# Optimization experiments

Measured on AMD Instinct MI355X. Metric: run time of the kernel, lower is better.

Reference implementation:

```python
import jax, jax.numpy as jnp
import numpy as np

B, T, C = 8, 2048, 1024
H, D = 16, 64
DLOW = 64  # D_DECAY = D_AAA = D_MV = D_GATE = 64
EPS_LN = 1e-5


def setup_inputs() -> dict:
    key = jax.random.key(0)
    ks = jax.random.split(key, 26)
    p = lambda k, shape, s=0.02: (jax.random.normal(k, shape, jnp.float32) * s)
    u = lambda k, shape: jax.random.uniform(k, shape, jnp.float32)
    return {
        "x":   jax.random.normal(ks[0], (B, T, C), jnp.float32),
        # token-shift mix coefficients (1,1,C)
        "x_r": u(ks[1], (1, 1, C)), "x_w": u(ks[2], (1, 1, C)),
        "x_k": u(ks[3], (1, 1, C)), "x_v": u(ks[4], (1, 1, C)),
        "x_a": u(ks[5], (1, 1, C)), "x_g": u(ks[6], (1, 1, C)),
        # decay lora: w1 [C,DLOW], w2 [DLOW,H], w0 [1,1,H,1]
        "w0": p(ks[7], (1, 1, H, 1)), "w1": p(ks[8], (C, DLOW)), "w2": p(ks[9], (DLOW, H)),
        # in-context lr lora
        "a0": p(ks[10], (1, 1, H, 1)), "a1": p(ks[11], (C, DLOW)), "a2": p(ks[12], (DLOW, H)),
        # value residual lora
        "v0": p(ks[13], (1, 1, C)), "v1": p(ks[14], (C, DLOW)), "v2": p(ks[15], (DLOW, C)),
        # gate lora
        "g1": p(ks[16], (C, DLOW)), "g2": p(ks[17], (DLOW, C)),
        "k_k": 0.85 + p(ks[18], (1, 1, C)),
        "r_k": p(ks[19], (H, D)),
        # main projections, stored [in, out] so x @ W matches nn.Linear
        "Wr": p(ks[20], (C, C)), "Wk": p(ks[21], (C, C)),
        "Wv": p(ks[22], (C, C)), "Wo": p(ks[23], (C, C)),
        # GroupNorm(n_head, n_embd) affine params
        "ln_w": jnp.ones((C,), jnp.float32) + p(ks[24], (C,)),
        "ln_b": p(ks[25], (C,)),
    }


def reference(x, x_r, x_w, x_k, x_v, x_a, x_g,
              w0, w1, w2, a0, a1, a2, v0, v1, v2, g1, g2,
              k_k, r_k, Wr, Wk, Wv, Wo, ln_w, ln_b):
    Bb, Tt, Cc = x.shape
    Hh, Dd = r_k.shape
    # token shift: sx = x_t - x_{t-1} (zero-padded)
    xx = jnp.concatenate([jnp.zeros((Bb, 1, Cc), x.dtype), x[:, :-1]], axis=1)
    sx = x - xx
    xr = x + sx * x_r
    xw = x + sx * x_w
    xk = x + sx * x_k
    xv = x + sx * x_v
    xa = x + sx * x_a
    xg = x + sx * x_g

    r = (xr @ Wr).reshape(Bb, Tt, Hh, Dd)
    # decay in (0, exp(-0.5)): exp(-softplus(-(w0 + lora)) - 0.5)
    w = jnp.exp(-jax.nn.softplus(-(w0 + (jnp.tanh(xw @ w1) @ w2).reshape(Bb, Tt, Hh, 1))) - 0.5)
    k = xk @ Wk
    v = xv @ Wv
    v_res_gate = jax.nn.sigmoid(v0 + jnp.tanh(xv @ v1) @ v2)
    v = v + (v - v) * v_res_gate  # no-op, kept for faithfulness
    a = jax.nn.sigmoid(a0 + (jnp.tanh(xa @ a1) @ a2).reshape(Bb, Tt, Hh, 1))
    g = jax.nn.sigmoid(jnp.tanh(xg @ g1) @ g2)

    kk = (k * k_k).reshape(Bb, Tt, Hh, Dd)
    kk = kk / jnp.maximum(jnp.linalg.norm(kk, axis=-1, keepdims=True), 1e-12)
    vh = v.reshape(Bb, Tt, Hh, Dd)

    # WKV linear recurrence: state = state * w_t + kk_t * v_t * a_t
    kv = (kk * vh * a).astype(jnp.float32)            # [B,T,H,D]
    w_t = jnp.moveaxis(w.astype(jnp.float32), 1, 0)   # [T,B,H,1]
    kv_t = jnp.moveaxis(kv, 1, 0)                     # [T,B,H,D]

    def step(state, inputs):
        wt, kvt = inputs
        state = state * wt + kvt
        return state, state

    init = jnp.zeros((Bb, Hh, Dd), jnp.float32)
    _, states = jax.lax.scan(step, init, (w_t, kv_t))  # [T,B,H,D]
    x_wkv = jnp.moveaxis(states, 0, 1).astype(x.dtype)  # [B,T,H,D]

    x_wkv = x_wkv * r
    bonus = jnp.sum(r * kk * r_k, axis=-1, keepdims=True) * vh
    x_wkv = x_wkv + bonus  # [B,T,H,D]

    # GroupNorm(H groups over C channels), per (B*T) sample
    mean = x_wkv.mean(axis=-1, keepdims=True)
    var = x_wkv.var(axis=-1, keepdims=True)
    xn = (x_wkv - mean) * jax.lax.rsqrt(var + EPS_LN)
    xn = xn.reshape(Bb, Tt, Cc) * ln_w + ln_b

    return (xn * g) @ Wo
```

## Files before the change

kernel.cpp:

```cpp
#include <hip/hip_runtime.h>


typedef __bf16 bf16;
typedef __attribute__((ext_vector_type(8))) __bf16 bf16x8;
typedef __attribute__((ext_vector_type(4))) float f32x4;

#define TBTOK 16384
#define TSEQ  2048
#define CDIM  1024
#define HN    16
#define CHUNK 32
#define NCH   64

__device__ __forceinline__ float wredsum(float v) {
#pragma unroll
  for (int o = 32; o > 0; o >>= 1) v += __shfl_xor(v, o, 64);
  return v;
}
__device__ __forceinline__ float redsum8(float v) {
#pragma unroll
  for (int o = 4; o > 0; o >>= 1) v += __shfl_xor(v, o, 64);
  return v;
}
__device__ __forceinline__ float sigmf(float x) { return 1.f / (1.f + expf(-x)); }

__device__ __forceinline__ void gl_lds16(const bf16* g, bf16* l) {
  __builtin_amdgcn_global_load_lds(
      (const __attribute__((address_space(1))) unsigned int*)g,
      (__attribute__((address_space(3))) unsigned int*)l, 16, 0, 0);
}

__global__ __launch_bounds__(256) void prep_kern(
    const float* __restrict__ x, const float* __restrict__ mr,
    const float* __restrict__ mk, const float* __restrict__ mv,
    bf16* __restrict__ xr, bf16* __restrict__ xk, bf16* __restrict__ xv,
    bf16* __restrict__ xbf,
    const float* __restrict__ Wr, const float* __restrict__ Wk,
    const float* __restrict__ Wv, const float* __restrict__ Wo,
    const float* __restrict__ w1, const float* __restrict__ a1, const float* __restrict__ g1,
    const float* __restrict__ mw, const float* __restrict__ ma, const float* __restrict__ mg,
    const float* __restrict__ g2, const float* __restrict__ w2, const float* __restrict__ a2,
    bf16* __restrict__ WrT, bf16* __restrict__ WkT, bf16* __restrict__ WvT, bf16* __restrict__ WoT,
    bf16* __restrict__ Bcat, bf16* __restrict__ g2T,
    bf16* __restrict__ w2T, bf16* __restrict__ a2T, float* __restrict__ zpad) {
  int bid0 = blockIdx.x;
  int tid = threadIdx.x;
  if (bid0 < 8192) {
    long i8 = ((long)bid0 * 256 + tid) * 8;
    int m = (int)(i8 >> 10);
    int c = (int)(i8 & 1023);
    f32x4 x0 = *(const f32x4*)(x + i8);
    f32x4 x1 = *(const f32x4*)(x + i8 + 4);
    f32x4 p0 = {0.f, 0.f, 0.f, 0.f}, p1 = {0.f, 0.f, 0.f, 0.f};
    if ((m & (TSEQ - 1)) != 0) {
      p0 = *(const f32x4*)(x + i8 - CDIM);
      p1 = *(const f32x4*)(x + i8 - CDIM + 4);
    }
    f32x4 r0 = *(const f32x4*)(mr + c), r1 = *(const f32x4*)(mr + c + 4);
    f32x4 k0 = *(const f32x4*)(mk + c), k1 = *(const f32x4*)(mk + c + 4);
    f32x4 v0 = *(const f32x4*)(mv + c), v1 = *(const f32x4*)(mv + c + 4);
    bf16x8 or_, ok_, ov_, ox_;
#pragma unroll
    for (int j = 0; j < 4; j++) {
      float s0 = x0[j] - p0[j], s1 = x1[j] - p1[j];
      or_[j] = (bf16)(x0[j] + s0 * r0[j]); or_[4 + j] = (bf16)(x1[j] + s1 * r1[j]);
      ok_[j] = (bf16)(x0[j] + s0 * k0[j]); ok_[4 + j] = (bf16)(x1[j] + s1 * k1[j]);
      ov_[j] = (bf16)(x0[j] + s0 * v0[j]); ov_[4 + j] = (bf16)(x1[j] + s1 * v1[j]);
      ox_[j] = (bf16)x0[j];                ox_[4 + j] = (bf16)x1[j];
    }
    *(bf16x8*)(xr + i8) = or_;
    *(bf16x8*)(xk + i8) = ok_;
    *(bf16x8*)(xv + i8) = ov_;
    *(bf16x8*)(xbf + i8) = ox_;
    return;
  }
  int bid = bid0 - 8192;
  int tx = tid & 31, ty = tid >> 5;
  __shared__ bf16 tile[32][33];
  if (bid < 4096) {
    int sel = bid >> 10, t = bid & 1023;
    int k0 = (t >> 5) * 32, n0 = (t & 31) * 32;
    const float* src = sel == 0 ? Wr : (sel == 1 ? Wk : (sel == 2 ? Wv : Wo));
    bf16* dst = sel == 0 ? WrT : (sel == 1 ? WkT : (sel == 2 ? WvT : WoT));
#pragma unroll
    for (int i = 0; i < 4; i++)
      tile[ty + i * 8][tx] = (bf16)src[(long)(k0 + ty + i * 8) * 1024 + n0 + tx];
    __syncthreads();
#pragma unroll
    for (int i = 0; i < 4; i++)
      dst[(long)(n0 + ty + i * 8) * 1024 + k0 + tx] = tile[tx][ty + i * 8];
  } else if (bid < 4480) {
    int idx = bid - 4096;
    int mat = idx >> 7, rem = idx & 127;
    int half = rem >> 6, t = rem & 63;
    int k0 = (t >> 1) * 32, n0 = (t & 1) * 32;
    const float* W = mat == 0 ? w1 : (mat == 1 ? a1 : g1);
    const float* mx = mat == 0 ? mw : (mat == 1 ? ma : mg);
#pragma unroll
    for (int i = 0; i < 4; i++) {
      int k = k0 + ty + i * 8;
      float s = half == 0 ? (1.f + mx[k]) : (-mx[k]);
      tile[ty + i * 8][tx] = (bf16)(s * W[(long)k * 64 + n0 + tx]);
    }
    __syncthreads();
#pragma unroll
    for (int i = 0; i < 4; i++)
      Bcat[(long)(mat * 64 + n0 + ty + i * 8) * 2048 + half * 1024 + k0 + tx] =
          tile[tx][ty + i * 8];
  } else if (bid < 4544) {
    int t = bid - 4480;
    int k0 = (t >> 5) * 32, n0 = (t & 31) * 32;
#pragma unroll
    for (int i = 0; i < 4; i++)
      tile[ty + i * 8][tx] = (bf16)g2[(long)(k0 + ty + i * 8) * 1024 + n0 + tx];
    __syncthreads();
#pragma unroll
    for (int i = 0; i < 4; i++)
      g2T[(long)(n0 + ty + i * 8) * 64 + k0 + tx] = tile[tx][ty + i * 8];
  } else {
#pragma unroll
    for (int rep = 0; rep < 4; rep++) {
      int idx = rep * 256 + tid;
      int k = idx >> 4, h = idx & 15;
      w2T[h * 64 + k] = (bf16)w2[idx];
      a2T[h * 64 + k] = (bf16)a2[idx];
    }
    if (tid < 64) zpad[tid] = 0.f;
  }
}

#define BARRIER __builtin_amdgcn_s_barrier()
#define LGKM0                                              \
  do {                                                     \
    asm volatile("s_waitcnt lgkmcnt(0)" ::: "memory");     \
    __builtin_amdgcn_sched_barrier(0);                     \
  } while (0)

#define READ_A(HALFP, QM)                                                                \
  {                                                                                      \
    const bf16* _h = (HALFP);                                                            \
    _Pragma("unroll") for (int i = 0; i < 4; i++) {                                      \
      int ra = (QM)*64 + i * 16 + lr;                                                    \
      _Pragma("unroll") for (int ks = 0; ks < 2; ks++)                                   \
          af[i][ks] = *(const bf16x8*)&_h[ra * 64 + (((ks * 4 + quad) ^ (ra & 7)) * 8)]; \
    }                                                                                    \
  }

#define READ_B(HALFP, QN)                                                                \
  {                                                                                      \
    const bf16* _h = (HALFP);                                                            \
    _Pragma("unroll") for (int jj = 0; jj < 2; jj++) {                                   \
      int rb = bro + ((QN)*2 + jj) * 16 + lr;                                            \
      _Pragma("unroll") for (int ks = 0; ks < 2; ks++)                                   \
          bfr[(QN)*2 + jj][ks] =                                                         \
              *(const bf16x8*)&_h[rb * 64 + (((ks * 4 + quad) ^ (rb & 7)) * 8)];         \
    }                                                                                    \
  }

#define MFMA16(QM, QN)                                                            \
  __builtin_amdgcn_s_setprio(1);                                                  \
  _Pragma("unroll") for (int ks = 0; ks < 2; ks++)                                \
  _Pragma("unroll") for (int i = 0; i < 4; i++)                                   \
  _Pragma("unroll") for (int jj = 0; jj < 2; jj++)                                \
      acc[(QM)*4 + i][(QN)*2 + jj] = __builtin_amdgcn_mfma_f32_16x16x32_bf16(     \
          af[i][ks], bfr[(QN)*2 + jj][ks], acc[(QM)*4 + i][(QN)*2 + jj], 0, 0, 0);\
  __builtin_amdgcn_s_setprio(0);

template <typename OT>
__global__ __launch_bounds__(512, 2) void gemm256_kern(
    const bf16* __restrict__ A0, const bf16* __restrict__ A1, const bf16* __restrict__ A2,
    const bf16* __restrict__ BT0, const bf16* __restrict__ BT1, const bf16* __restrict__ BT2,
    OT* __restrict__ out0, OT* __restrict__ out1, OT* __restrict__ out2,
    int K, int nbpm) {
  int nwg = gridDim.x;
  int id = blockIdx.x;
  int qq = nwg >> 3;
  int wg = (id & 7) * qq + (id >> 3);
  int mat = wg / nbpm;
  int rem = wg - mat * nbpm;
  int m0 = (rem & 63) << 8;
  int n0 = (rem >> 6) << 8;
  const bf16* Am = mat == 0 ? A0 : (mat == 1 ? A1 : A2);
  const bf16* BTm = mat == 0 ? BT0 : (mat == 1 ? BT1 : BT2);
  OT* out = mat == 0 ? out0 : (mat == 1 ? out1 : out2);

  __shared__ bf16 Al[2][2][128 * 64];
  __shared__ bf16 Bl[2][2][128 * 64];

  int tid = threadIdx.x;
  int w = tid >> 6, lane = tid & 63, quad = lane >> 4, lr = lane & 15;
  int wr = w >> 2, wc = w & 3;
  int hb = wc >> 1, bro = (wc & 1) * 64;

  int swz = ((tid & 7) ^ ((tid >> 3) & 7)) * 8;
  const bf16* aBase = Am + (long)(m0 + (tid >> 3)) * K + swz;
  const bf16* bBase = BTm + (long)(n0 + (tid >> 3)) * K + swz;

  auto stgA = [&](int db, int h, int t) {
    const bf16* g = aBase + (long)(h * 128) * K + t * 64;
    bf16* l = &Al[db][h][0] + w * 512;
    gl_lds16(g, l);
    gl_lds16(g + (long)64 * K, l + 4096);
  };
  auto stgB = [&](int db, int h, int t) {
    const bf16* g = bBase + (long)(h * 128) * K + t * 64;
    bf16* l = &Bl[db][h][0] + w * 512;
    gl_lds16(g, l);
    gl_lds16(g + (long)64 * K, l + 4096);
  };

  const bf16* A0p = &Al[0][wr][0];
  const bf16* A1p = &Al[1][wr][0];
  const bf16* B0p = &Bl[0][hb][0];
  const bf16* B1p = &Bl[1][hb][0];

  f32x4 acc[8][4] = {};
  bf16x8 af[4][2], bfr[4][2];

  int NT = K >> 6, NU = NT >> 1;

  stgB(0, 0, 0); stgA(0, 0, 0); stgA(0, 1, 0); stgB(0, 1, 0);
  stgB(1, 0, 1); stgA(1, 0, 1);
  asm volatile("s_waitcnt vmcnt(4)" ::: "memory");
  BARRIER;

#pragma unroll 1
  for (int u = 0; u < NU; u++) {
    int t1 = 2 * u + 1, t2 = 2 * u + 2, t3 = 2 * u + 3;
    READ_A(A0p, 0);
    READ_B(B0p, 0);
    stgA(1, 1, t1);
    asm volatile("s_waitcnt lgkmcnt(8)" ::: "memory");
    BARRIER; LGKM0;
    MFMA16(0, 0);
    BARRIER;
    READ_B(B0p, 1);
    stgB(1, 1, t1);
    BARRIER; LGKM0;
    MFMA16(0, 1);
    BARRIER;
    READ_A(A0p, 1);
    if (t2 < NT) stgB(0, 0, t2);
    BARRIER; LGKM0;
    MFMA16(1, 1);
    BARRIER;
    if (t2 < NT) stgA(0, 0, t2);
    BARRIER;
    __builtin_amdgcn_sched_barrier(0);
    MFMA16(1, 0);
    if (t2 < NT) { asm volatile("s_waitcnt vmcnt(4)" ::: "memory"); }
    else         { asm volatile("s_waitcnt vmcnt(0)" ::: "memory"); }
    BARRIER;
    READ_A(A1p, 0);
    READ_B(B1p, 0);
    if (t2 < NT) stgA(0, 1, t2);
    asm volatile("s_waitcnt lgkmcnt(8)" ::: "memory");
    BARRIER; LGKM0;
    MFMA16(0, 0);
    BARRIER;
    READ_B(B1p, 1);
    if (t2 < NT) stgB(0, 1, t2);
    BARRIER; LGKM0;
    MFMA16(0, 1);
    BARRIER;
    READ_A(A1p, 1);
    if (t3 < NT) stgB(1, 0, t3);
    BARRIER; LGKM0;
    MFMA16(1, 1);
    BARRIER;
    if (t3 < NT) stgA(1, 0, t3);
    BARRIER;
    __builtin_amdgcn_sched_barrier(0);
    MFMA16(1, 0);
    if (t3 < NT) { asm volatile("s_waitcnt vmcnt(4)" ::: "memory"); }
    else         { asm volatile("s_waitcnt vmcnt(0)" ::: "memory"); }
    BARRIER;
  }

#pragma unroll
  for (int i = 0; i < 8; i++)
#pragma unroll
    for (int j = 0; j < 4; j++)
#pragma unroll
      for (int rg = 0; rg < 4; rg++) {
        int row = m0 + wr * 128 + i * 16 + quad * 4 + rg;
        int col = n0 + wc * 64 + j * 16 + lr;
        out[(long)row * CDIM + col] = (OT)acc[i][j][rg];
      }
}

__global__ __launch_bounds__(256) void stage1_kern(
    const bf16* __restrict__ xbf, const bf16* __restrict__ Bcat,
    const float* __restrict__ zpad, const bf16* __restrict__ w2T, const bf16* __restrict__ a2T,
    const float* __restrict__ w0, const float* __restrict__ a0,
    bf16* __restrict__ t1g, float* __restrict__ w_arr, float* __restrict__ a_arr) {
  int m0 = blockIdx.x * 64;
  int part = blockIdx.y;
  __shared__ bf16 Al[64 * 32];
  __shared__ bf16 Bl[128 * 32];
  __shared__ bf16 Lt1[64 * 136];

  int tid = threadIdx.x;
  int w = tid >> 6, lane = tid & 63, quad = lane >> 4, lr = lane & 15;
  int wm = w * 16;

  int r0 = tid >> 2, kc0 = (tid & 3) * 8;
  int m = m0 + r0;
  const bf16* asrc = xbf + (long)m * CDIM + kc0;
  bool firstrow = (m & (TSEQ - 1)) == 0;
  const bf16* psrc = firstrow ? (const bf16*)zpad : xbf + (long)(m - 1) * CDIM + kc0;
  int pstep = firstrow ? 0 : 32;
  int brow0 = part ? 128 : 0;
  const bf16* bs0 = Bcat + (long)(brow0 + r0) * 2048 + kc0;
  const bf16* bs1 = bs0 + (long)64 * 2048;
  bf16* la = Al + w * 512;
  bf16* lb0 = Bl + w * 512;
  bf16* lb1 = Bl + 2048 + w * 512;

  if (part == 0) {
    f32x4 acc[8] = {};
#pragma unroll 1
    for (int kk = 0; kk < 64; kk++) {
      if (kk < 32) { gl_lds16(asrc, la); asrc += 32; }
      else         { gl_lds16(psrc, la); psrc += pstep; }
      gl_lds16(bs0, lb0);
      gl_lds16(bs1, lb1);
      bs0 += 32; bs1 += 32;
      __syncthreads();
      bf16x8 af = *(const bf16x8*)&Al[(wm + lr) * 32 + quad * 8];
#pragma unroll
      for (int nf = 0; nf < 8; nf++) {
        bf16x8 bff = *(const bf16x8*)&Bl[(nf * 16 + lr) * 32 + quad * 8];
        acc[nf] = __builtin_amdgcn_mfma_f32_16x16x32_bf16(af, bff, acc[nf], 0, 0, 0);
      }
      __syncthreads();
    }
#pragma unroll
    for (int nf = 0; nf < 8; nf++)
#pragma unroll
      for (int rg = 0; rg < 4; rg++) {
        int row = wm + quad * 4 + rg;
        Lt1[row * 136 + nf * 16 + lr] = (bf16)tanhf(acc[nf][rg]);
      }
    __syncthreads();
#pragma unroll
    for (int rep = 0; rep < 4; rep++) {
      int idx = rep * 256 + tid;
      int row = idx >> 4, h = idx & 15;
      const bf16* rw = &Lt1[row * 136];
      const bf16* ra = rw + 64;
      const bf16* ww = w2T + h * 64;
      const bf16* aw = a2T + h * 64;
      float dw = 0.f, da = 0.f;
#pragma unroll
      for (int k = 0; k < 64; k++) {
        dw += (float)rw[k] * (float)ww[k];
        da += (float)ra[k] * (float)aw[k];
      }
      w_arr[h * TBTOK + m0 + row] = 0.60653066f * sigmf(w0[h] + dw);
      a_arr[h * TBTOK + m0 + row] = sigmf(a0[h] + da);
    }
  } else {
    f32x4 acc[4] = {};
#pragma unroll 1
    for (int kk = 0; kk < 64; kk++) {
      if (kk < 32) { gl_lds16(asrc, la); asrc += 32; }
      else         { gl_lds16(psrc, la); psrc += pstep; }
      gl_lds16(bs0, lb0);
      bs0 += 32;
      __syncthreads();
      bf16x8 af = *(const bf16x8*)&Al[(wm + lr) * 32 + quad * 8];
#pragma unroll
      for (int nf = 0; nf < 4; nf++) {
        bf16x8 bff = *(const bf16x8*)&Bl[(nf * 16 + lr) * 32 + quad * 8];
        acc[nf] = __builtin_amdgcn_mfma_f32_16x16x32_bf16(af, bff, acc[nf], 0, 0, 0);
      }
      __syncthreads();
    }
#pragma unroll
    for (int nf = 0; nf < 4; nf++)
#pragma unroll
      for (int rg = 0; rg < 4; rg++) {
        int row = wm + quad * 4 + rg;
        t1g[(long)(m0 + row) * 64 + nf * 16 + lr] = (bf16)tanhf(acc[nf][rg]);
      }
  }
}

__global__ __launch_bounds__(256) void scan1_kern(
    const bf16* __restrict__ k_buf, const bf16* __restrict__ v_buf, const bf16* __restrict__ r_buf,
    const float* __restrict__ k_k, const float* __restrict__ r_k,
    const float* __restrict__ a_arr, const float* __restrict__ w_arr,
    float* __restrict__ kv2, float* __restrict__ Parr, float* __restrict__ bonus,
    float* __restrict__ Lend) {
  int wid = blockIdx.x * 4 + (threadIdx.x >> 6);
  int lane = threadIdx.x & 63;
  int bh = wid >> 6, c = wid & 63;
  int b = bh >> 4, h = bh & 15;
  int mstart = b * TSEQ + c * CHUNK;
  int kc = h * 64 + lane;
  float kkc = k_k[kc], rkc = r_k[kc];
  float st = 0.f, cw = 1.f;
  long mbase = (long)mstart * CDIM + kc;
  int hm = h * TBTOK + mstart;
  long sbase = ((long)hm) * 64 + lane;
  float kf = (float)k_buf[mbase] * kkc;
  float vf = (float)v_buf[mbase];
  float rf = (float)r_buf[mbase];
  float af = a_arr[hm];
  float wt = w_arr[hm];
  for (int t = 0; t < CHUNK; t++) {
    float kf_n = 0.f, vf_n = 0.f, rf_n = 0.f, af_n = 0.f, wt_n = 0.f;
    if (t < CHUNK - 1) {
      kf_n = (float)k_buf[mbase + CDIM] * kkc;
      vf_n = (float)v_buf[mbase + CDIM];
      rf_n = (float)r_buf[mbase + CDIM];
      af_n = a_arr[hm + 1];
      wt_n = w_arr[hm + 1];
    }
    float ss = wredsum(kf * kf);
    float kkn = kf / fmaxf(sqrtf(ss), 1e-12f);
    st = st * wt + kkn * vf * af;
    kv2[sbase] = st;
    cw *= wt;
    float bs = wredsum(rf * kkn * rkc);
    if (lane == 0) {
      Parr[hm] = cw;
      bonus[(mstart + t) * HN + h] = bs;
    }
    kf = kf_n; vf = vf_n; rf = rf_n; af = af_n; wt = wt_n;
    mbase += CDIM; hm += 1; sbase += 64;
  }
  Lend[(long)wid * 64 + lane] = st;
}

__global__ __launch_bounds__(256) void gate_post_kern(
    const bf16* __restrict__ t1g, const bf16* __restrict__ g2T,
    const float* __restrict__ kv2, const float* __restrict__ Parr,
    const float* __restrict__ Lend, const float* __restrict__ bonus,
    bf16* __restrict__ r_buf, const bf16* __restrict__ v_buf,
    const float* __restrict__ ln_w, const float* __restrict__ ln_b) {
  int ncol0 = blockIdx.x * 128;
  int m0 = blockIdx.y * 128;

  __shared__ bf16 Al[128 * 32];
  __shared__ bf16 Bl[128 * 32];
  __shared__ bf16 gtile[128 * 136];

  int tid = threadIdx.x;
  int w = tid >> 6, lane = tid & 63, quad = lane >> 4, lr = lane & 15;
  int wm = (w & 1) * 64, wn = (w >> 1) * 64;

  f32x4 acc[4][4] = {};

  int r0 = tid >> 2, kc0 = (tid & 3) * 8;
  const bf16* ag0 = t1g + (long)(m0 + r0) * 64 + kc0;
  const bf16* ag1 = ag0 + (long)64 * 64;
  const bf16* bg0 = g2T + (long)(ncol0 + r0) * 64 + kc0;
  const bf16* bg1 = bg0 + (long)64 * 64;
  bf16* la0 = Al + w * 512;
  bf16* la1 = Al + 2048 + w * 512;
  bf16* lb0 = Bl + w * 512;
  bf16* lb1 = Bl + 2048 + w * 512;

  for (int k0 = 0; k0 < 64; k0 += 32) {
    gl_lds16(ag0, la0);
    gl_lds16(ag1, la1);
    gl_lds16(bg0, lb0);
    gl_lds16(bg1, lb1);
    ag0 += 32; ag1 += 32; bg0 += 32; bg1 += 32;
    __syncthreads();
    bf16x8 af[4], bff[4];
#pragma unroll
    for (int i = 0; i < 4; i++) af[i] = *(const bf16x8*)&Al[(wm + i * 16 + lr) * 32 + quad * 8];
#pragma unroll
    for (int j = 0; j < 4; j++) bff[j] = *(const bf16x8*)&Bl[(wn + j * 16 + lr) * 32 + quad * 8];
#pragma unroll
    for (int i = 0; i < 4; i++)
#pragma unroll
      for (int j = 0; j < 4; j++)
        acc[i][j] = __builtin_amdgcn_mfma_f32_16x16x32_bf16(af[i], bff[j], acc[i][j], 0, 0, 0);
    __syncthreads();
  }
#pragma unroll
  for (int i = 0; i < 4; i++)
#pragma unroll
    for (int j = 0; j < 4; j++)
#pragma unroll
      for (int rg = 0; rg < 4; rg++) {
        int row = wm + i * 16 + quad * 4 + rg;
        int col = wn + j * 16 + lr;
        gtile[row * 136 + col] = (bf16)sigmf(acc[i][j][rg]);
      }
  __syncthreads();

  int c_loc = (tid & 15) * 8;
  int col_g = ncol0 + c_loc;
  int h = col_g >> 6;
  int d0 = col_g & 63;
  f32x4 lnw0 = *(const f32x4*)(ln_w + col_g);
  f32x4 lnw1 = *(const f32x4*)(ln_w + col_g + 4);
  f32x4 lnb0 = *(const f32x4*)(ln_b + col_g);
  f32x4 lnb1 = *(const f32x4*)(ln_b + col_g + 4);
#pragma unroll
  for (int jj = 0; jj < 8; jj++) {
    int row = jj * 16 + (tid >> 4);
    int row_g = m0 + row;
    int b = row_g >> 11;
    int ch = (row_g & (TSEQ - 1)) >> 5;
    long kvb = ((long)h * TBTOK + row_g) * 64 + d0;
    f32x4 st0 = *(const f32x4*)(kv2 + kvb);
    f32x4 st1 = *(const f32x4*)(kv2 + kvb + 4);
    f32x4 cy0 = {0.f, 0.f, 0.f, 0.f}, cy1 = {0.f, 0.f, 0.f, 0.f};
    if (ch != 0) {
      long lb = ((long)((b * 16 + h) * NCH + ch - 1)) * 64 + d0;
      cy0 = *(const f32x4*)(Lend + lb);
      cy1 = *(const f32x4*)(Lend + lb + 4);
    }
    float pw = Parr[h * TBTOK + row_g];
    float bs = bonus[row_g * HN + h];
    long rb = (long)row_g * CDIM + col_g;
    bf16x8 rf8 = *(const bf16x8*)(r_buf + rb);
    bf16x8 vf8 = *(const bf16x8*)(v_buf + rb);
    bf16x8 g8 = *(const bf16x8*)&gtile[row * 136 + c_loc];
    float xw[8];
#pragma unroll
    for (int q = 0; q < 4; q++) {
      xw[q]     = (st0[q] + pw * cy0[q]) * (float)rf8[q]     + bs * (float)vf8[q];
      xw[4 + q] = (st1[q] + pw * cy1[q]) * (float)rf8[4 + q] + bs * (float)vf8[4 + q];
    }
    float sum = 0.f;
#pragma unroll
    for (int q = 0; q < 8; q++) sum += xw[q];
    float mn = redsum8(sum) * (1.f / 64.f);
    float vs = 0.f;
#pragma unroll
    for (int q = 0; q < 8; q++) {
      xw[q] -= mn;
      vs += xw[q] * xw[q];
    }
    float var = redsum8(vs) * (1.f / 64.f);
    float rq = rsqrtf(var + 1e-5f);
    bf16x8 o8;
#pragma unroll
    for (int q = 0; q < 4; q++) {
      o8[q]     = (bf16)((xw[q] * rq * lnw0[q] + lnb0[q]) * (float)g8[q]);
      o8[4 + q] = (bf16)((xw[4 + q] * rq * lnw1[q] + lnb1[q]) * (float)g8[4 + q]);
    }
    *(bf16x8*)(r_buf + rb) = o8;
  }
}

extern "C" void kernel_launch(void* const* d_in, const int* in_sizes, int n_in,
                              void* d_out, int out_size, void* d_ws, size_t ws_size,
                              hipStream_t stream) {
  const float* x    = (const float*)d_in[0];
  const float* x_r  = (const float*)d_in[1];
  const float* x_w  = (const float*)d_in[2];
  const float* x_k  = (const float*)d_in[3];
  const float* x_v  = (const float*)d_in[4];
  const float* x_a  = (const float*)d_in[5];
  const float* x_g  = (const float*)d_in[6];
  const float* w0   = (const float*)d_in[7];
  const float* w1   = (const float*)d_in[8];
  const float* w2   = (const float*)d_in[9];
  const float* a0   = (const float*)d_in[10];
  const float* a1   = (const float*)d_in[11];
  const float* a2   = (const float*)d_in[12];
  const float* g1   = (const float*)d_in[16];
  const float* g2   = (const float*)d_in[17];
  const float* k_k  = (const float*)d_in[18];
  const float* r_k  = (const float*)d_in[19];
  const float* Wr   = (const float*)d_in[20];
  const float* Wk   = (const float*)d_in[21];
  const float* Wv   = (const float*)d_in[22];
  const float* Wo   = (const float*)d_in[23];
  const float* ln_w = (const float*)d_in[24];
  const float* ln_b = (const float*)d_in[25];
  float* out = (float*)d_out;

  char* p = (char*)d_ws;
  auto carve = [&](size_t bytes) {
    void* r = (void*)p;
    p += (bytes + 255) & ~(size_t)255;
    return r;
  };
  bf16* WrT = (bf16*)carve(1024 * 1024 * 2);
  bf16* WkT = (bf16*)carve(1024 * 1024 * 2);
  bf16* WvT = (bf16*)carve(1024 * 1024 * 2);
  bf16* WoT = (bf16*)carve(1024 * 1024 * 2);
  bf16* Bcat = (bf16*)carve(192 * 2048 * 2);
  bf16* g2T  = (bf16*)carve(1024 * 64 * 2);
  bf16* w2T  = (bf16*)carve(16 * 64 * 2);
  bf16* a2T  = (bf16*)carve(16 * 64 * 2);
  float* zpad = (float*)carve(64 * 4);
  bf16* t1g   = (bf16*)carve((size_t)TBTOK * 64 * 2);
  bf16* r_buf = (bf16*)carve((size_t)TBTOK * CDIM * 2);
  bf16* k_buf = (bf16*)carve((size_t)TBTOK * CDIM * 2);
  bf16* v_buf = (bf16*)carve((size_t)TBTOK * CDIM * 2);
  float* w_arr = (float*)carve((size_t)TBTOK * HN * 4);
  float* a_arr = (float*)carve((size_t)TBTOK * HN * 4);
  float* bonus = (float*)carve((size_t)TBTOK * HN * 4);
  float* Parr  = (float*)carve((size_t)TBTOK * HN * 4);
  float* Lend  = (float*)carve((size_t)128 * NCH * 64 * 4);
  bf16* xr  = (bf16*)carve((size_t)TBTOK * CDIM * 2);
  bf16* xk  = (bf16*)carve((size_t)TBTOK * CDIM * 2);
  bf16* xv  = (bf16*)carve((size_t)TBTOK * CDIM * 2);
  bf16* xbf = (bf16*)carve((size_t)TBTOK * CDIM * 2);
  float* kv2 = (float*)xv;

  prep_kern<<<dim3(8192 + 4545), 256, 0, stream>>>(
      x, x_r, x_k, x_v, xr, xk, xv, xbf,
      Wr, Wk, Wv, Wo, w1, a1, g1, x_w, x_a, x_g, g2, w2, a2,
      WrT, WkT, WvT, WoT, Bcat, g2T, w2T, a2T, zpad);
  stage1_kern<<<dim3(TBTOK / 64, 2), 256, 0, stream>>>(
      xbf, Bcat, zpad, w2T, a2T, w0, a0, t1g, w_arr, a_arr);
  gemm256_kern<bf16><<<dim3(768), 512, 0, stream>>>(
      xr, xk, xv, WrT, WkT, WvT, r_buf, k_buf, v_buf, 1024, 256);
  scan1_kern<<<dim3(128 * NCH / 4), 256, 0, stream>>>(
      k_buf, v_buf, r_buf, k_k, r_k, a_arr, w_arr, kv2, Parr, bonus, Lend);
  gate_post_kern<<<dim3(8, TBTOK / 128), 256, 0, stream>>>(
      t1g, g2T, kv2, Parr, Lend, bonus, r_buf, v_buf, ln_w, ln_b);
  gemm256_kern<float><<<dim3(256), 512, 0, stream>>>(
      r_buf, r_buf, r_buf, WoT, WoT, WoT, out, out, out, 1024, 256);
}
```

Measured before the change: 553.3 us.

## Merge stage1 LoRA parts into one triple-buffered swizzled GEMM and regroup gemm256 prefetches

The stage1 kernel no longer splits into two grid halves. Each block now computes all 192 LoRA output columns over a 64-wide K tile, using a three-stage LDS ring buffer with XOR-swizzled layouts, a larger per-warp MFMA tile and raised wave priority during the MFMA burst. This halves the number of times the A operand is re-read and replaces a fully synchronous, barrier-per-step loop with prefetching. Separately, the main gemm256 loop now issues all of a tile's A/B half-loads together one stage earlier, with deeper vmcnt waits. The cost is more LDS per block (lower occupancy) and fewer stage1 blocks.

```diff
diff --git a/kernel.cpp b/kernel.cpp
--- a/kernel.cpp
+++ b/kernel.cpp
@@ -219,60 +219,56 @@
 
   int NT = K >> 6, NU = NT >> 1;
 
-  stgB(0, 0, 0); stgA(0, 0, 0); stgA(0, 1, 0); stgB(0, 1, 0);
-  stgB(1, 0, 1); stgA(1, 0, 1);
-  asm volatile("s_waitcnt vmcnt(4)" ::: "memory");
+  stgB(0, 0, 0); stgB(0, 1, 0); stgA(0, 0, 0); stgA(0, 1, 0);
+  stgB(1, 0, 1); stgB(1, 1, 1); stgA(1, 0, 1); stgA(1, 1, 1);
+  asm volatile("s_waitcnt vmcnt(8)" ::: "memory");
   BARRIER;
 
 #pragma unroll 1
   for (int u = 0; u < NU; u++) {
-    int t1 = 2 * u + 1, t2 = 2 * u + 2, t3 = 2 * u + 3;
+    int t2 = 2 * u + 2, t3 = 2 * u + 3;
     READ_A(A0p, 0);
     READ_B(B0p, 0);
-    stgA(1, 1, t1);
     asm volatile("s_waitcnt lgkmcnt(8)" ::: "memory");
     BARRIER; LGKM0;
     MFMA16(0, 0);
     BARRIER;
     READ_B(B0p, 1);
-    stgB(1, 1, t1);
     BARRIER; LGKM0;
     MFMA16(0, 1);
     BARRIER;
     READ_A(A0p, 1);
-    if (t2 < NT) stgB(0, 0, t2);
+    if (t2 < NT) { stgB(0, 0, t2); stgB(0, 1, t2); }
     BARRIER; LGKM0;
     MFMA16(1, 1);
     BARRIER;
-    if (t2 < NT) stgA(0, 0, t2);
+    if (t2 < NT) { stgA(0, 0, t2); stgA(0, 1, t2); }
     BARRIER;
     __builtin_amdgcn_sched_barrier(0);
     MFMA16(1, 0);
-    if (t2 < NT) { asm volatile("s_waitcnt vmcnt(4)" ::: "memory"); }
+    if (t2 < NT) { asm volatile("s_waitcnt vmcnt(8)" ::: "memory"); }
     else         { asm volatile("s_waitcnt vmcnt(0)" ::: "memory"); }
     BARRIER;
     READ_A(A1p, 0);
     READ_B(B1p, 0);
-    if (t2 < NT) stgA(0, 1, t2);
     asm volatile("s_waitcnt lgkmcnt(8)" ::: "memory");
     BARRIER; LGKM0;
     MFMA16(0, 0);
     BARRIER;
     READ_B(B1p, 1);
-    if (t2 < NT) stgB(0, 1, t2);
     BARRIER; LGKM0;
     MFMA16(0, 1);
     BARRIER;
     READ_A(A1p, 1);
-    if (t3 < NT) stgB(1, 0, t3);
+    if (t3 < NT) { stgB(1, 0, t3); stgB(1, 1, t3); }
     BARRIER; LGKM0;
     MFMA16(1, 1);
     BARRIER;
-    if (t3 < NT) stgA(1, 0, t3);
+    if (t3 < NT) { stgA(1, 0, t3); stgA(1, 1, t3); }
     BARRIER;
     __builtin_amdgcn_sched_barrier(0);
     MFMA16(1, 0);
-    if (t3 < NT) { asm volatile("s_waitcnt vmcnt(4)" ::: "memory"); }
+    if (t3 < NT) { asm volatile("s_waitcnt vmcnt(8)" ::: "memory"); }
     else         { asm volatile("s_waitcnt vmcnt(0)" ::: "memory"); }
     BARRIER;
   }
@@ -295,95 +291,117 @@
     const float* __restrict__ w0, const float* __restrict__ a0,
     bf16* __restrict__ t1g, float* __restrict__ w_arr, float* __restrict__ a_arr) {
   int m0 = blockIdx.x * 64;
-  int part = blockIdx.y;
-  __shared__ bf16 Al[64 * 32];
-  __shared__ bf16 Bl[128 * 32];
+  __shared__ bf16 Abuf[3][64 * 64];
+  __shared__ bf16 Bbuf[3][192 * 64];
   __shared__ bf16 Lt1[64 * 136];
 
   int tid = threadIdx.x;
   int w = tid >> 6, lane = tid & 63, quad = lane >> 4, lr = lane & 15;
-  int wm = w * 16;
-
-  int r0 = tid >> 2, kc0 = (tid & 3) * 8;
-  int m = m0 + r0;
-  const bf16* asrc = xbf + (long)m * CDIM + kc0;
-  bool firstrow = (m & (TSEQ - 1)) == 0;
-  const bf16* psrc = firstrow ? (const bf16*)zpad : xbf + (long)(m - 1) * CDIM + kc0;
-  int pstep = firstrow ? 0 : 32;
-  int brow0 = part ? 128 : 0;
-  const bf16* bs0 = Bcat + (long)(brow0 + r0) * 2048 + kc0;
-  const bf16* bs1 = bs0 + (long)64 * 2048;
-  bf16* la = Al + w * 512;
-  bf16* lb0 = Bl + w * 512;
-  bf16* lb1 = Bl + 2048 + w * 512;
-
-  if (part == 0) {
-    f32x4 acc[8] = {};
+
+  int r0 = tid >> 3, s0 = tid & 7;
+  int c0 = (s0 ^ (r0 & 7)) * 8;
+  const bf16* arow0 = xbf + (long)(m0 + r0) * CDIM + c0;
+  const bf16* arow1 = xbf + (long)(m0 + 32 + r0) * CDIM + c0;
+  bool fr0 = ((m0 + r0) & (TSEQ - 1)) == 0;
+  const bf16* aprev0 = fr0 ? ((const bf16*)zpad) : (arow0 - CDIM);
+  const bf16* aprev1 = arow1 - CDIM;
+  long pm0 = fr0 ? 0 : 64;
+  const bf16* brow = Bcat + (long)r0 * 2048 + c0;
+
+  bf16* sA0 = &Abuf[0][0]; bf16* sA1 = &Abuf[1][0]; bf16* sA2 = &Abuf[2][0];
+  bf16* sB0 = &Bbuf[0][0]; bf16* sB1 = &Bbuf[1][0]; bf16* sB2 = &Bbuf[2][0];
+
+  auto stage = [&](bf16* sA, bf16* sB, int kk) {
+    const bf16* a0s = (kk < 16) ? (arow0 + kk * 64) : (aprev0 + (long)(kk - 16) * pm0);
+    const bf16* a1s = (kk < 16) ? (arow1 + kk * 64) : (aprev1 + (long)(kk - 16) * 64);
+    gl_lds16(a0s, sA + w * 512);
+    gl_lds16(a1s, sA + 2048 + w * 512);
+    const bf16* bs = brow + kk * 64;
+#pragma unroll
+    for (int j = 0; j < 6; j++)
+      gl_lds16(bs + (long)j * 32 * 2048, sB + j * 2048 + w * 512);
+  };
+
+  f32x4 acc[4][3] = {};
+
+  stage(sA0, sB0, 0);
+  stage(sA1, sB1, 1);
+  stage(sA2, sB2, 2);
+  asm volatile("s_waitcnt vmcnt(16)" ::: "memory");
+  BARRIER;
+
 #pragma unroll 1
-    for (int kk = 0; kk < 64; kk++) {
-      if (kk < 32) { gl_lds16(asrc, la); asrc += 32; }
-      else         { gl_lds16(psrc, la); psrc += pstep; }
-      gl_lds16(bs0, lb0);
-      gl_lds16(bs1, lb1);
-      bs0 += 32; bs1 += 32;
-      __syncthreads();
-      bf16x8 af = *(const bf16x8*)&Al[(wm + lr) * 32 + quad * 8];
-#pragma unroll
-      for (int nf = 0; nf < 8; nf++) {
-        bf16x8 bff = *(const bf16x8*)&Bl[(nf * 16 + lr) * 32 + quad * 8];
-        acc[nf] = __builtin_amdgcn_mfma_f32_16x16x32_bf16(af, bff, acc[nf], 0, 0, 0);
+  for (int t = 0; t < 32; t++) {
+    bf16x8 af[4][2], bfr[3][2];
+#pragma unroll
+    for (int i = 0; i < 4; i++) {
+      int ra = i * 16 + lr;
+#pragma unroll
+      for (int ks = 0; ks < 2; ks++)
+        af[i][ks] = *(const bf16x8*)&sA0[ra * 64 + (((ks * 4 + quad) ^ (ra & 7)) * 8)];
+    }
+#pragma unroll
+    for (int n = 0; n < 3; n++) {
+      int rb = w * 48 + n * 16 + lr;
+#pragma unroll
+      for (int ks = 0; ks < 2; ks++)
+        bfr[n][ks] = *(const bf16x8*)&sB0[rb * 64 + (((ks * 4 + quad) ^ (rb & 7)) * 8)];
+    }
+    LGKM0;
+    __builtin_amdgcn_s_setprio(1);
+#pragma unroll
+    for (int ks = 0; ks < 2; ks++)
+#pragma unroll
+      for (int i = 0; i < 4; i++)
+#pragma unroll
+        for (int n = 0; n < 3; n++)
+          acc[i][n] = __builtin_amdgcn_mfma_f32_16x16x32_bf16(af[i][ks], bfr[n][ks],
+                                                              acc[i][n], 0, 0, 0);
+    __builtin_amdgcn_s_setprio(0);
+    BARRIER;
+    if (t + 3 < 32) {
+      stage(sA0, sB0, t + 3);
+      asm volatile("s_waitcnt vmcnt(16)" ::: "memory");
+    } else if (t == 29) {
+      asm volatile("s_waitcnt vmcnt(8)" ::: "memory");
+    } else if (t == 30) {
+      asm volatile("s_waitcnt vmcnt(0)" ::: "memory");
+    }
+    BARRIER;
+    bf16* tmpA = sA0; sA0 = sA1; sA1 = sA2; sA2 = tmpA;
+    bf16* tmpB = sB0; sB0 = sB1; sB1 = sB2; sB2 = tmpB;
+  }
+
+#pragma unroll
+  for (int i = 0; i < 4; i++)
+#pragma unroll
+    for (int n = 0; n < 3; n++) {
+      int col = w * 48 + n * 16 + lr;
+#pragma unroll
+      for (int rg = 0; rg < 4; rg++) {
+        int row = i * 16 + quad * 4 + rg;
+        float tv = tanhf(acc[i][n][rg]);
+        if (col < 128) Lt1[row * 136 + col] = (bf16)tv;
+        else t1g[(long)(m0 + row) * 64 + (col - 128)] = (bf16)tv;
       }
-      __syncthreads();
-    }
-#pragma unroll
-    for (int nf = 0; nf < 8; nf++)
-#pragma unroll
-      for (int rg = 0; rg < 4; rg++) {
-        int row = wm + quad * 4 + rg;
-        Lt1[row * 136 + nf * 16 + lr] = (bf16)tanhf(acc[nf][rg]);
-      }
-    __syncthreads();
-#pragma unroll
-    for (int rep = 0; rep < 4; rep++) {
-      int idx = rep * 256 + tid;
-      int row = idx >> 4, h = idx & 15;
-      const bf16* rw = &Lt1[row * 136];
-      const bf16* ra = rw + 64;
-      const bf16* ww = w2T + h * 64;
-      const bf16* aw = a2T + h * 64;
-      float dw = 0.f, da = 0.f;
-#pragma unroll
-      for (int k = 0; k < 64; k++) {
-        dw += (float)rw[k] * (float)ww[k];
-        da += (float)ra[k] * (float)aw[k];
-      }
-      w_arr[h * TBTOK + m0 + row] = 0.60653066f * sigmf(w0[h] + dw);
-      a_arr[h * TBTOK + m0 + row] = sigmf(a0[h] + da);
-    }
-  } else {
-    f32x4 acc[4] = {};
-#pragma unroll 1
-    for (int kk = 0; kk < 64; kk++) {
-      if (kk < 32) { gl_lds16(asrc, la); asrc += 32; }
-      else         { gl_lds16(psrc, la); psrc += pstep; }
-      gl_lds16(bs0, lb0);
-      bs0 += 32;
-      __syncthreads();
-      bf16x8 af = *(const bf16x8*)&Al[(wm + lr) * 32 + quad * 8];
-#pragma unroll
-      for (int nf = 0; nf < 4; nf++) {
-        bf16x8 bff = *(const bf16x8*)&Bl[(nf * 16 + lr) * 32 + quad * 8];
-        acc[nf] = __builtin_amdgcn_mfma_f32_16x16x32_bf16(af, bff, acc[nf], 0, 0, 0);
-      }
-      __syncthreads();
-    }
-#pragma unroll
-    for (int nf = 0; nf < 4; nf++)
-#pragma unroll
-      for (int rg = 0; rg < 4; rg++) {
-        int row = wm + quad * 4 + rg;
-        t1g[(long)(m0 + row) * 64 + nf * 16 + lr] = (bf16)tanhf(acc[nf][rg]);
-      }
+    }
+  __syncthreads();
+#pragma unroll
+  for (int rep = 0; rep < 4; rep++) {
+    int idx = rep * 256 + tid;
+    int row = idx >> 4, h = idx & 15;
+    const bf16* rw = &Lt1[row * 136];
+    const bf16* ra = rw + 64;
+    const bf16* ww = w2T + h * 64;
+    const bf16* aw = a2T + h * 64;
+    float dw = 0.f, da = 0.f;
+#pragma unroll
+    for (int k = 0; k < 64; k++) {
+      dw += (float)rw[k] * (float)ww[k];
+      da += (float)ra[k] * (float)aw[k];
+    }
+    w_arr[h * TBTOK + m0 + row] = 0.60653066f * sigmf(w0[h] + dw);
+    a_arr[h * TBTOK + m0 + row] = sigmf(a0[h] + da);
   }
 }
 
@@ -613,7 +631,7 @@
       x, x_r, x_k, x_v, xr, xk, xv, xbf,
       Wr, Wk, Wv, Wo, w1, a1, g1, x_w, x_a, x_g, g2, w2, a2,
       WrT, WkT, WvT, WoT, Bcat, g2T, w2T, a2T, zpad);
-  stage1_kern<<<dim3(TBTOK / 64, 2), 256, 0, stream>>>(
+  stage1_kern<<<dim3(TBTOK / 64), 256, 0, stream>>>(
       xbf, Bcat, zpad, w2T, a2T, w0, a0, t1g, w_arr, a_arr);
   gemm256_kern<bf16><<<dim3(768), 512, 0, stream>>>(
       xr, xk, xv, WrT, WkT, WvT, r_buf, k_buf, v_buf, 1024, 256);
```

Measured after the change: 517.7 us. 1.07x faster.
